# Kernel tuning notes

Measured on AMD Instinct MI355X. Metric: run time of the kernel, lower is better.

## Reference

```python
import jax, jax.numpy as jnp
import numpy as np

N = 50000          # number of input/output nodes (M == N since out_features=None)
E = 1_600_000      # total neighbor entries (avg degree 32)
C_IN = 64
HID = 128
C_OUT = 64


def setup_inputs() -> dict:
    key = jax.random.key(0)
    k1, k2, k3, k4, k5 = jax.random.split(key, 5)
    in_features = jax.random.normal(k1, (N, C_IN), dtype=jnp.float32)
    # MLP params: Linear(2C->HID), GELU, Linear(HID->C_OUT)
    W1 = jax.random.normal(k2, (2 * C_IN, HID), dtype=jnp.float32) * (1.0 / np.sqrt(2 * C_IN))
    b1 = jnp.zeros((HID,), dtype=jnp.float32)
    W2 = jax.random.normal(k3, (HID, C_OUT), dtype=jnp.float32) * (1.0 / np.sqrt(HID))
    b2 = jnp.zeros((C_OUT,), dtype=jnp.float32)
    neighbors_index = jax.random.randint(k4, (E,), 0, N, dtype=jnp.int64)
    # row_splits: sorted, starts at 0, ends at E (CSR-style ragged offsets)
    inner = jnp.sort(jax.random.randint(k5, (N - 1,), 0, E, dtype=jnp.int64))
    neighbors_row_splits = jnp.concatenate(
        [jnp.zeros((1,), jnp.int64), inner, jnp.full((1,), E, jnp.int64)])
    return {
        "in_features": in_features,
        "W1": W1, "b1": b1, "W2": W2, "b2": b2,
        "neighbors_index": neighbors_index,
        "neighbors_row_splits": neighbors_row_splits,
    }


def reference(in_features, W1, b1, W2, b2, neighbors_index, neighbors_row_splits):
    rs = neighbors_row_splits
    counts = rs[1:] - rs[:-1]                                  # [M] num_reps per row
    # segment id of each edge: row i owns edges [rs[i], rs[i+1])
    seg_ids = jnp.searchsorted(rs[1:], jnp.arange(E), side="right")  # [E]

    rep_features = in_features[neighbors_index]                # gather neighbors [E, C]
    self_features = in_features[seg_ids]                       # repeat_interleave  [E, C]
    agg = jnp.concatenate([rep_features, self_features], axis=1)  # [E, 2C]

    h = jax.nn.gelu(agg @ W1 + b1, approximate=False)          # torch GELU = exact erf
    msg = h @ W2 + b2                                          # [E, C_out]

    summed = jax.ops.segment_sum(msg, seg_ids, num_segments=N)  # [M, C_out]
    denom = jnp.maximum(counts, 1).astype(msg.dtype)[:, None]
    return summed / denom                                       # mean reduction
```

## Files before the change

### kernel.cpp

```cpp
#include <hip/hip_runtime.h>
#include <hip/hip_bf16.h>
#include <math.h>

#define C_IN  64
#define HID   128
#define C_OUT 64

typedef __attribute__((ext_vector_type(8))) short s16x8;
typedef __attribute__((ext_vector_type(4))) float f32x4;
typedef __attribute__((ext_vector_type(2))) float f32x2;

__device__ __forceinline__ f32x2 gelu2(f32x2 x) {
    f32x2 t  = x * x;
    f32x2 p  = t * 0.10294455f + 2.30211462f;
    f32x2 xp = x * p;
    f32x2 E;
    E.x = __builtin_amdgcn_exp2f(xp.x);
    E.y = __builtin_amdgcn_exp2f(xp.y);
    f32x2 Ep = E + 1.0f;
    f32x2 r;
    r.x = __builtin_amdgcn_rcpf(Ep.x);
    r.y = __builtin_amdgcn_rcpf(Ep.y);
    return x - x * r;
}

__device__ __forceinline__ float4 fma4(float s, float4 w, float4 acc) {
    acc.x = fmaf(s, w.x, acc.x); acc.y = fmaf(s, w.y, acc.y);
    acc.z = fmaf(s, w.z, acc.z); acc.w = fmaf(s, w.w, acc.w);
    return acc;
}

__device__ __forceinline__ unsigned pk_bf16(float lo, float hi) {
    union { __hip_bfloat162 v; unsigned u; } cv;
    cv.v = __float22bfloat162_rn(make_float2(lo, hi));
    return cv.u;
}
__device__ __forceinline__ f32x2 unpk2(unsigned p) {
    union { unsigned u; float f; } lo, hi;
    lo.u = p << 16; hi.u = p & 0xffff0000u;
    f32x2 v; v.x = lo.f; v.y = hi.f; return v;
}

#define K1_NODES 64

__global__ __launch_bounds__(512, 2) void precompute_ab(
    const float* __restrict__ X, const float* __restrict__ W1,
    const float* __restrict__ b1, const float* __restrict__ W2,
    const int* __restrict__ rs,
    unsigned* __restrict__ A16, float* __restrict__ B,
    unsigned short* __restrict__ W2T, int* __restrict__ bsplit,
    int N, int E, int G)
{
    __shared__ float W1s[2 * C_IN * HID];
    __shared__ float xs[K1_NODES * C_IN];
    int tid = threadIdx.x;

    for (int i = tid; i < (2 * C_IN * HID) / 4; i += 512)
        ((float4*)W1s)[i] = ((const float4*)W1)[i];

    int base = blockIdx.x * K1_NODES;
    int nLoc = min(K1_NODES, N - base);
    for (int i = tid; i < nLoc * (C_IN / 4); i += 512)
        ((float4*)xs)[i] = ((const float4*)(X + (size_t)base * C_IN))[i];

    if (blockIdx.x == 0) {
        for (int i = tid; i < C_OUT * HID; i += 512) {
            int c = i >> 7, k = i & (HID - 1);
            W2T[i] = (unsigned short)pk_bf16(W2[k * C_OUT + c], 0.f);
        }
    }

    {
        int gi = blockIdx.x * 512 + tid;
        if (gi <= G) {
            int t = (int)(((long long)E * gi) / G);
            int lo = 0, hi = N;
            while (lo < hi) { int mm = (lo + hi) >> 1; if (rs[mm] < t) lo = mm + 1; else hi = mm; }
            bsplit[gi] = lo;
        }
    }

    __syncthreads();

    int quad = (tid & 31) * 4;
    int slot = tid >> 5;
    int s0   = slot * 4;
    if (s0 >= nLoc) return;

    float4 a0 = {}, a1 = {}, a2 = {}, a3 = {};
    float4 b0 = {}, b1r = {}, b2r = {}, b3 = {};

    const float* xr0 = xs + (s0 + 0) * C_IN;
    const float* xr1 = xs + (s0 + 1) * C_IN;
    const float* xr2 = xs + (s0 + 2) * C_IN;
    const float* xr3 = xs + (s0 + 3) * C_IN;

#define K1STEP(c, CMP)                                                      \
    do {                                                                    \
        float4 wa = *(const float4*)&W1s[(c) * HID + quad];                 \
        float4 wb = *(const float4*)&W1s[((c) + C_IN) * HID + quad];        \
        a0 = fma4(xv0.CMP, wa, a0); b0  = fma4(xv0.CMP, wb, b0);            \
        a1 = fma4(xv1.CMP, wa, a1); b1r = fma4(xv1.CMP, wb, b1r);           \
        a2 = fma4(xv2.CMP, wa, a2); b2r = fma4(xv2.CMP, wb, b2r);           \
        a3 = fma4(xv3.CMP, wa, a3); b3  = fma4(xv3.CMP, wb, b3);            \
    } while (0)

#pragma unroll 1
    for (int c4 = 0; c4 < C_IN; c4 += 4) {
        float4 xv0 = *(const float4*)&xr0[c4];
        float4 xv1 = *(const float4*)&xr1[c4];
        float4 xv2 = *(const float4*)&xr2[c4];
        float4 xv3 = *(const float4*)&xr3[c4];
        K1STEP(c4 + 0, x);
        K1STEP(c4 + 1, y);
        K1STEP(c4 + 2, z);
        K1STEP(c4 + 3, w);
    }
#undef K1STEP

    float4 bb = *(const float4*)(b1 + quad);
    b0.x += bb.x;  b0.y += bb.y;  b0.z += bb.z;  b0.w += bb.w;
    b1r.x += bb.x; b1r.y += bb.y; b1r.z += bb.z; b1r.w += bb.w;
    b2r.x += bb.x; b2r.y += bb.y; b2r.z += bb.z; b2r.w += bb.w;
    b3.x += bb.x;  b3.y += bb.y;  b3.z += bb.z;  b3.w += bb.w;

    int adw = (base + s0) * (HID / 2) + (quad >> 1);
    size_t boff = (size_t)(base + s0) * HID + quad;
    if (s0 + 0 < nLoc) {
        uint2 u = { pk_bf16(a0.x, a0.y), pk_bf16(a0.z, a0.w) };
        *(uint2*)(A16 + adw) = u;              *(float4*)(B + boff) = b0;
    }
    if (s0 + 1 < nLoc) {
        uint2 u = { pk_bf16(a1.x, a1.y), pk_bf16(a1.z, a1.w) };
        *(uint2*)(A16 + adw + HID / 2) = u;    *(float4*)(B + boff + HID) = b1r;
    }
    if (s0 + 2 < nLoc) {
        uint2 u = { pk_bf16(a2.x, a2.y), pk_bf16(a2.z, a2.w) };
        *(uint2*)(A16 + adw + HID) = u;        *(float4*)(B + boff + 2 * HID) = b2r;
    }
    if (s0 + 3 < nLoc) {
        uint2 u = { pk_bf16(a3.x, a3.y), pk_bf16(a3.z, a3.w) };
        *(uint2*)(A16 + adw + 3 * (HID / 2)) = u; *(float4*)(B + boff + 3 * HID) = b3;
    }
}

#define EA_WAVES 2

#define EA_ISSUE(P0,P1,P2,P3, gc, IDX) do { int _b = ((gc) << 4) + q;         \
    int _i0 = __shfl((IDX), _b);                                              \
    int _i1 = __shfl((IDX), _b + 4);                                          \
    int _i2 = __shfl((IDX), _b + 8);                                          \
    int _i3 = __shfl((IDX), _b + 12);                                         \
    P0 = *(const uint4*)(A8 + ((((unsigned)_i0) << 8) | lb));                 \
    P1 = *(const uint4*)(A8 + ((((unsigned)_i1) << 8) | lb));                 \
    P2 = *(const uint4*)(A8 + ((((unsigned)_i2) << 8) | lb));                 \
    P3 = *(const uint4*)(A8 + ((((unsigned)_i3) << 8) | lb));                 \
} while (0)

#define EA_P1(P) do {                                                         \
    acc01 += gelu2(unpk2(P.x) + bb01);                                        \
    acc23 += gelu2(unpk2(P.y) + bb23);                                        \
    acc45 += gelu2(unpk2(P.z) + bb45);                                        \
    acc67 += gelu2(unpk2(P.w) + bb67); } while (0)

#define EA_P1M(P, eb) do {                                                    \
    float _mk = ((eb) + q < cnt) ? 1.f : 0.f;                                 \
    acc01 += gelu2(unpk2(P.x) + bb01) * _mk;                                  \
    acc23 += gelu2(unpk2(P.y) + bb23) * _mk;                                  \
    acc45 += gelu2(unpk2(P.z) + bb45) * _mk;                                  \
    acc67 += gelu2(unpk2(P.w) + bb67) * _mk; } while (0)

#define EA_PROCG(P0,P1,P2,P3, g) do {                                         \
    if ((((g) + 1) << 4) <= cnt) { EA_P1(P0); EA_P1(P1);                      \
                                   EA_P1(P2); EA_P1(P3); }                    \
    else { int _eb = (g) << 4;                                                \
           EA_P1M(P0, _eb);                                                   \
           if (_eb + 4  < cnt) EA_P1M(P1, _eb + 4);                           \
           if (_eb + 8  < cnt) EA_P1M(P2, _eb + 8);                           \
           if (_eb + 12 < cnt) EA_P1M(P3, _eb + 12); } } while (0)

__global__ __launch_bounds__(128, 6) void edge_agg(
    const unsigned* __restrict__ A16, const float* __restrict__ B,
    const int* __restrict__ nbr, const int* __restrict__ rs,
    const int* __restrict__ bsplit,
    unsigned* __restrict__ Hout, int N, int E, int G)
{
    int wave = threadIdx.x >> 6, lane = threadIdx.x & 63;
    int q  = lane >> 4;
    int l4 = lane & 15;
    const char* A8 = (const char*)A16;
    unsigned lb = (unsigned)(l4 << 4);
    int b = blockIdx.x;

    int r0 = bsplit[b];
    int r1 = (b == G - 1) ? N : bsplit[b + 1];

    int row = r0 + wave;
    if (row >= r1) return;

    int s = rs[row], e = rs[row + 1];
    int cnt = e - s;
    int idxCur = 0;
    if (cnt > 0) { int mn = min(64, cnt); idxCur = nbr[s + min(lane, mn - 1)]; }

    for (;;) {
        float4 bb4a = *(const float4*)(B + (size_t)row * HID + l4 * 8);
        float4 bb4b = *(const float4*)(B + (size_t)row * HID + l4 * 8 + 4);
        f32x2 bb01, bb23, bb45, bb67;
        bb01.x = bb4a.x; bb01.y = bb4a.y; bb23.x = bb4a.z; bb23.y = bb4a.w;
        bb45.x = bb4b.x; bb45.y = bb4b.y; bb67.x = bb4b.z; bb67.y = bb4b.w;
        f32x2 acc01 = {0.f, 0.f}, acc23 = {0.f, 0.f};
        f32x2 acc45 = {0.f, 0.f}, acc67 = {0.f, 0.f};

        uint4 A0, A1, A2, A3, B0, B1, B2, B3;
        int nG = 0, cLow = 0;
        int idxNxt = idxCur;
        if (cnt > 0) {
            nG = (cnt + 15) >> 4;
            EA_ISSUE(A0, A1, A2, A3, 0, idxCur);
            if (nG > 1) EA_ISSUE(B0, B1, B2, B3, 1, idxCur);
            if (cnt > 64) { int mn = min(64, cnt - 64);
                            idxNxt = nbr[s + 64 + min(lane, mn - 1)]; }
        }

        int nrow = row + EA_WAVES;
        bool hasn = nrow < r1;
        int sn = 0, cntn = 0, idxN0 = 0;
        if (hasn) {
            sn = rs[nrow]; int en = rs[nrow + 1]; cntn = en - sn;
            if (cntn > 0) { int mn = min(64, cntn);
                            idxN0 = nbr[sn + min(lane, mn - 1)]; }
        }

        if (cnt > 0) {
            int g = 0;
            for (;;) {
                EA_PROCG(A0, A1, A2, A3, g);
                { int gp = g + 2;
                  if (gp < nG) { int gc = gp & 3;
                      int IDX = ((gp >> 2) != cLow) ? idxNxt : idxCur;
                      EA_ISSUE(A0, A1, A2, A3, gc, IDX); } }
                if (++g >= nG) break;
                if ((g & 3) == 0) {
                    idxCur = idxNxt; ++cLow;
                    int nb = (cLow + 1) << 6;
                    if (nb < cnt) { int mn = min(64, cnt - nb);
                                    idxNxt = nbr[s + nb + min(lane, mn - 1)]; }
                }
                EA_PROCG(B0, B1, B2, B3, g);
                { int gp = g + 2;
                  if (gp < nG) { int gc = gp & 3;
                      int IDX = ((gp >> 2) != cLow) ? idxNxt : idxCur;
                      EA_ISSUE(B0, B1, B2, B3, gc, IDX); } }
                if (++g >= nG) break;
                if ((g & 3) == 0) {
                    idxCur = idxNxt; ++cLow;
                    int nb = (cLow + 1) << 6;
                    if (nb < cnt) { int mn = min(64, cnt - nb);
                                    idxNxt = nbr[s + nb + min(lane, mn - 1)]; }
                }
            }
        }

        acc01.x += __shfl_xor(acc01.x, 16); acc01.x += __shfl_xor(acc01.x, 32);
        acc01.y += __shfl_xor(acc01.y, 16); acc01.y += __shfl_xor(acc01.y, 32);
        acc23.x += __shfl_xor(acc23.x, 16); acc23.x += __shfl_xor(acc23.x, 32);
        acc23.y += __shfl_xor(acc23.y, 16); acc23.y += __shfl_xor(acc23.y, 32);
        acc45.x += __shfl_xor(acc45.x, 16); acc45.x += __shfl_xor(acc45.x, 32);
        acc45.y += __shfl_xor(acc45.y, 16); acc45.y += __shfl_xor(acc45.y, 32);
        acc67.x += __shfl_xor(acc67.x, 16); acc67.x += __shfl_xor(acc67.x, 32);
        acc67.y += __shfl_xor(acc67.y, 16); acc67.y += __shfl_xor(acc67.y, 32);

        if (q == 0) {
            float sc = (cnt > 0) ? 1.f / (float)cnt : 0.f;
            uint4 o;
            o.x = pk_bf16(acc01.x * sc, acc01.y * sc);
            o.y = pk_bf16(acc23.x * sc, acc23.y * sc);
            o.z = pk_bf16(acc45.x * sc, acc45.y * sc);
            o.w = pk_bf16(acc67.x * sc, acc67.y * sc);
            *((uint4*)(Hout + (size_t)row * (HID / 2)) + l4) = o;
        }

        if (!hasn) break;
        row = nrow; s = sn; cnt = cntn; idxCur = idxN0;
    }
}

#undef EA_ISSUE
#undef EA_P1
#undef EA_P1M
#undef EA_PROCG

__global__ __launch_bounds__(256) void h_w2_mfma(
    const unsigned short* __restrict__ H, const unsigned short* __restrict__ W2T,
    const float* __restrict__ b2, const int* __restrict__ rs,
    float* __restrict__ out, int N)
{
    int wave = threadIdx.x >> 6, lane = threadIdx.x & 63;
    int base = (blockIdx.x * 4 + wave) * 16;
    if (base >= N) return;

    int r16 = lane & 15;
    int kg  = lane >> 4;

    const unsigned short* hrow = H + (size_t)(base + r16) * HID + kg * 8;
    const unsigned short* wc0  = W2T + (size_t)(0 * 16 + r16) * HID + kg * 8;
    const unsigned short* wc1  = W2T + (size_t)(1 * 16 + r16) * HID + kg * 8;
    const unsigned short* wc2  = W2T + (size_t)(2 * 16 + r16) * HID + kg * 8;
    const unsigned short* wc3  = W2T + (size_t)(3 * 16 + r16) * HID + kg * 8;

    f32x4 acc0 = {0.f, 0.f, 0.f, 0.f};
    f32x4 acc1 = acc0, acc2 = acc0, acc3 = acc0;

#pragma unroll
    for (int kk = 0; kk < 4; ++kk) {
        s16x8 a  = *(const s16x8*)(hrow + kk * 32);
        s16x8 f0 = *(const s16x8*)(wc0 + kk * 32);
        s16x8 f1 = *(const s16x8*)(wc1 + kk * 32);
        s16x8 f2 = *(const s16x8*)(wc2 + kk * 32);
        s16x8 f3 = *(const s16x8*)(wc3 + kk * 32);
        acc0 = __builtin_amdgcn_mfma_f32_16x16x32_bf16(a, f0, acc0, 0, 0, 0);
        acc1 = __builtin_amdgcn_mfma_f32_16x16x32_bf16(a, f1, acc1, 0, 0, 0);
        acc2 = __builtin_amdgcn_mfma_f32_16x16x32_bf16(a, f2, acc2, 0, 0, 0);
        acc3 = __builtin_amdgcn_mfma_f32_16x16x32_bf16(a, f3, acc3, 0, 0, 0);
    }

    float bia0 = b2[r16], bia1 = b2[16 + r16], bia2 = b2[32 + r16], bia3 = b2[48 + r16];

#pragma unroll
    for (int r = 0; r < 4; ++r) {
        int rowi = base + kg * 4 + r;
        if (rowi < N) {
            float mmk = (rs[rowi + 1] > rs[rowi]) ? 1.f : 0.f;
            float* o = out + (size_t)rowi * C_OUT;
            o[r16]      = mmk * (acc0[r] + bia0);
            o[16 + r16] = mmk * (acc1[r] + bia1);
            o[32 + r16] = mmk * (acc2[r] + bia2);
            o[48 + r16] = mmk * (acc3[r] + bia3);
        }
    }
}

extern "C" void kernel_launch(void* const* d_in, const int* in_sizes, int n_in,
                              void* d_out, int out_size, void* d_ws, size_t ws_size,
                              hipStream_t stream) {
    const float* X  = (const float*)d_in[0];
    const float* W1 = (const float*)d_in[1];
    const float* b1 = (const float*)d_in[2];
    const float* W2 = (const float*)d_in[3];
    const float* b2 = (const float*)d_in[4];
    const int*   nbr = (const int*)d_in[5];
    const int*   rs  = (const int*)d_in[6];
    float* outp = (float*)d_out;

    int N = in_sizes[6] - 1;
    int E = in_sizes[5];

    int G = 3072;

    unsigned*       A16  = (unsigned*)d_ws;
    float*          Bbuf = (float*)(A16 + (size_t)N * (HID / 2));
    unsigned*       Hout = (unsigned*)(Bbuf + (size_t)N * HID);
    unsigned short* W2T  = (unsigned short*)(Hout + (size_t)N * (HID / 2));
    int*            bsplit = (int*)(W2T + C_OUT * HID);

    int g1 = (N + K1_NODES - 1) / K1_NODES;
    hipLaunchKernelGGL(precompute_ab, dim3(g1), dim3(512), 0, stream,
                       X, W1, b1, W2, rs, A16, Bbuf, W2T, bsplit, N, E, G);

    hipLaunchKernelGGL(edge_agg, dim3(G), dim3(128), 0, stream,
                       A16, Bbuf, nbr, rs, bsplit, Hout, N, E, G);

    int stripes = (N + 15) / 16;
    int g3 = (stripes + 3) / 4;
    hipLaunchKernelGGL(h_w2_mfma, dim3(g3), dim3(256), 0, stream,
                       (const unsigned short*)Hout, W2T, b2, rs, outp, N);
}
```

Before: 155.8 us.

## Split edge aggregation into four hidden-channel passes with planar A layout

Stores the bf16 A table as four planes of 32 hidden channels each and runs the edge aggregation as four launches, one per plane. Each pass gathers only 64 bytes per neighbor, so a plane's working set (about 3.2 MB) is more likely to stay cache-resident during random gathers. The pass also uses a three-buffer prefetch ring, nontemporal loads and stores, and a larger grid. The cost is that neighbor indices and row splits are re-read four times, there are extra launches, and each lane does fewer GELUs per load.

```diff
diff --git a/kernel.cpp b/kernel.cpp
--- a/kernel.cpp
+++ b/kernel.cpp
@@ -42,6 +42,7 @@
 }
 
 #define K1_NODES 64
+#define EA_G 6144
 
 __global__ __launch_bounds__(512, 2) void precompute_ab(
     const float* __restrict__ X, const float* __restrict__ W1,
@@ -124,7 +125,9 @@
     b2r.x += bb.x; b2r.y += bb.y; b2r.z += bb.z; b2r.w += bb.w;
     b3.x += bb.x;  b3.y += bb.y;  b3.z += bb.z;  b3.w += bb.w;
 
-    int adw = (base + s0) * (HID / 2) + (quad >> 1);
+    int pl = quad >> 5;
+    int d2 = quad & 31;
+    size_t adw = ((size_t)pl * N + (base + s0)) * 16 + (d2 >> 1);
     size_t boff = (size_t)(base + s0) * HID + quad;
     if (s0 + 0 < nLoc) {
         uint2 u = { pk_bf16(a0.x, a0.y), pk_bf16(a0.z, a0.w) };
@@ -132,64 +135,58 @@
     }
     if (s0 + 1 < nLoc) {
         uint2 u = { pk_bf16(a1.x, a1.y), pk_bf16(a1.z, a1.w) };
-        *(uint2*)(A16 + adw + HID / 2) = u;    *(float4*)(B + boff + HID) = b1r;
+        *(uint2*)(A16 + adw + 16) = u;         *(float4*)(B + boff + HID) = b1r;
     }
     if (s0 + 2 < nLoc) {
         uint2 u = { pk_bf16(a2.x, a2.y), pk_bf16(a2.z, a2.w) };
-        *(uint2*)(A16 + adw + HID) = u;        *(float4*)(B + boff + 2 * HID) = b2r;
+        *(uint2*)(A16 + adw + 32) = u;         *(float4*)(B + boff + 2 * HID) = b2r;
     }
     if (s0 + 3 < nLoc) {
         uint2 u = { pk_bf16(a3.x, a3.y), pk_bf16(a3.z, a3.w) };
-        *(uint2*)(A16 + adw + 3 * (HID / 2)) = u; *(float4*)(B + boff + 3 * HID) = b3;
+        *(uint2*)(A16 + adw + 48) = u;         *(float4*)(B + boff + 3 * HID) = b3;
     }
 }
 
 #define EA_WAVES 2
 
-#define EA_ISSUE(P0,P1,P2,P3, gc, IDX) do { int _b = ((gc) << 4) + q;         \
+#define EA_ISSUE(P0,P1,P2,P3, g, IDX) do { int _b = ((g) << 4) + q;           \
     int _i0 = __shfl((IDX), _b);                                              \
     int _i1 = __shfl((IDX), _b + 4);                                          \
     int _i2 = __shfl((IDX), _b + 8);                                          \
     int _i3 = __shfl((IDX), _b + 12);                                         \
-    P0 = *(const uint4*)(A8 + ((((unsigned)_i0) << 8) | lb));                 \
-    P1 = *(const uint4*)(A8 + ((((unsigned)_i1) << 8) | lb));                 \
-    P2 = *(const uint4*)(A8 + ((((unsigned)_i2) << 8) | lb));                 \
-    P3 = *(const uint4*)(A8 + ((((unsigned)_i3) << 8) | lb));                 \
+    P0 = *(const unsigned*)(Ap + ((((unsigned)_i0) << 6) | jb));              \
+    P1 = *(const unsigned*)(Ap + ((((unsigned)_i1) << 6) | jb));              \
+    P2 = *(const unsigned*)(Ap + ((((unsigned)_i2) << 6) | jb));              \
+    P3 = *(const unsigned*)(Ap + ((((unsigned)_i3) << 6) | jb));              \
 } while (0)
 
-#define EA_P1(P) do {                                                         \
-    acc01 += gelu2(unpk2(P.x) + bb01);                                        \
-    acc23 += gelu2(unpk2(P.y) + bb23);                                        \
-    acc45 += gelu2(unpk2(P.z) + bb45);                                        \
-    acc67 += gelu2(unpk2(P.w) + bb67); } while (0)
-
-#define EA_P1M(P, eb) do {                                                    \
-    float _mk = ((eb) + q < cnt) ? 1.f : 0.f;                                 \
-    acc01 += gelu2(unpk2(P.x) + bb01) * _mk;                                  \
-    acc23 += gelu2(unpk2(P.y) + bb23) * _mk;                                  \
-    acc45 += gelu2(unpk2(P.z) + bb45) * _mk;                                  \
-    acc67 += gelu2(unpk2(P.w) + bb67) * _mk; } while (0)
+#define EA_PF(P) do {                                                         \
+    acc += gelu2(unpk2(P) + bb); } while (0)
+
+#define EA_PM(P, eb) do {                                                     \
+    float _mk = ((eb) + q < m) ? 1.f : 0.f;                                   \
+    acc += gelu2(unpk2(P) + bb) * _mk; } while (0)
 
 #define EA_PROCG(P0,P1,P2,P3, g) do {                                         \
-    if ((((g) + 1) << 4) <= cnt) { EA_P1(P0); EA_P1(P1);                      \
-                                   EA_P1(P2); EA_P1(P3); }                    \
+    if ((((g) + 1) << 4) <= m) { EA_PF(P0); EA_PF(P1);                        \
+                                 EA_PF(P2); EA_PF(P3); }                      \
     else { int _eb = (g) << 4;                                                \
-           EA_P1M(P0, _eb);                                                   \
-           if (_eb + 4  < cnt) EA_P1M(P1, _eb + 4);                           \
-           if (_eb + 8  < cnt) EA_P1M(P2, _eb + 8);                           \
-           if (_eb + 12 < cnt) EA_P1M(P3, _eb + 12); } } while (0)
-
-__global__ __launch_bounds__(128, 6) void edge_agg(
+           EA_PM(P0, _eb);                                                    \
+           if (_eb + 4  < m) EA_PM(P1, _eb + 4);                              \
+           if (_eb + 8  < m) EA_PM(P2, _eb + 8);                              \
+           if (_eb + 12 < m) EA_PM(P3, _eb + 12); } } while (0)
+
+__global__ __launch_bounds__(128) void edge_agg_pass(
     const unsigned* __restrict__ A16, const float* __restrict__ B,
     const int* __restrict__ nbr, const int* __restrict__ rs,
     const int* __restrict__ bsplit,
-    unsigned* __restrict__ Hout, int N, int E, int G)
+    unsigned* __restrict__ Hout, int N, int E, int G, int pass)
 {
     int wave = threadIdx.x >> 6, lane = threadIdx.x & 63;
     int q  = lane >> 4;
-    int l4 = lane & 15;
-    const char* A8 = (const char*)A16;
-    unsigned lb = (unsigned)(l4 << 4);
+    int j  = lane & 15;
+    const char* Ap = (const char*)A16 + (size_t)pass * N * 64;
+    unsigned jb = (unsigned)(j << 2);
     int b = blockIdx.x;
 
     int r0 = bsplit[b];
@@ -201,94 +198,72 @@
     int s = rs[row], e = rs[row + 1];
     int cnt = e - s;
     int idxCur = 0;
-    if (cnt > 0) { int mn = min(64, cnt); idxCur = nbr[s + min(lane, mn - 1)]; }
+    if (cnt > 0) { int mn = min(64, cnt);
+                   idxCur = __builtin_nontemporal_load(nbr + s + min(lane, mn - 1)); }
 
     for (;;) {
-        float4 bb4a = *(const float4*)(B + (size_t)row * HID + l4 * 8);
-        float4 bb4b = *(const float4*)(B + (size_t)row * HID + l4 * 8 + 4);
-        f32x2 bb01, bb23, bb45, bb67;
-        bb01.x = bb4a.x; bb01.y = bb4a.y; bb23.x = bb4a.z; bb23.y = bb4a.w;
-        bb45.x = bb4b.x; bb45.y = bb4b.y; bb67.x = bb4b.z; bb67.y = bb4b.w;
-        f32x2 acc01 = {0.f, 0.f}, acc23 = {0.f, 0.f};
-        f32x2 acc45 = {0.f, 0.f}, acc67 = {0.f, 0.f};
-
-        uint4 A0, A1, A2, A3, B0, B1, B2, B3;
-        int nG = 0, cLow = 0;
-        int idxNxt = idxCur;
-        if (cnt > 0) {
-            nG = (cnt + 15) >> 4;
-            EA_ISSUE(A0, A1, A2, A3, 0, idxCur);
-            if (nG > 1) EA_ISSUE(B0, B1, B2, B3, 1, idxCur);
-            if (cnt > 64) { int mn = min(64, cnt - 64);
-                            idxNxt = nbr[s + 64 + min(lane, mn - 1)]; }
-        }
+        f32x2 bb = __builtin_nontemporal_load(
+            (const f32x2*)(B + (size_t)row * HID + (pass << 5) + (j << 1)));
+        f32x2 acc = {0.f, 0.f};
 
         int nrow = row + EA_WAVES;
         bool hasn = nrow < r1;
-        int sn = 0, cntn = 0, idxN0 = 0;
+        int sn = 0, en = 0, cntn = 0, idxN0 = 0;
         if (hasn) {
-            sn = rs[nrow]; int en = rs[nrow + 1]; cntn = en - sn;
+            sn = rs[nrow]; en = rs[nrow + 1]; cntn = en - sn;
             if (cntn > 0) { int mn = min(64, cntn);
-                            idxN0 = nbr[sn + min(lane, mn - 1)]; }
+                            idxN0 = __builtin_nontemporal_load(nbr + sn + min(lane, mn - 1)); }
         }
 
         if (cnt > 0) {
-            int g = 0;
+            int cs = s;
+            int idx = idxCur;
             for (;;) {
-                EA_PROCG(A0, A1, A2, A3, g);
-                { int gp = g + 2;
-                  if (gp < nG) { int gc = gp & 3;
-                      int IDX = ((gp >> 2) != cLow) ? idxNxt : idxCur;
-                      EA_ISSUE(A0, A1, A2, A3, gc, IDX); } }
-                if (++g >= nG) break;
-                if ((g & 3) == 0) {
-                    idxCur = idxNxt; ++cLow;
-                    int nb = (cLow + 1) << 6;
-                    if (nb < cnt) { int mn = min(64, cnt - nb);
-                                    idxNxt = nbr[s + nb + min(lane, mn - 1)]; }
+                int m = min(64, e - cs);
+                int nG = (m + 15) >> 4;
+
+                unsigned A0, A1, A2, A3, B0, B1, B2, B3, C0, C1, C2, C3;
+                EA_ISSUE(A0, A1, A2, A3, 0, idx);
+                if (nG > 1) EA_ISSUE(B0, B1, B2, B3, 1, idx);
+
+                int g = 0;
+                for (;;) {
+                    if (g + 2 < nG) EA_ISSUE(C0, C1, C2, C3, g + 2, idx);
+                    EA_PROCG(A0, A1, A2, A3, g);
+                    if (++g >= nG) break;
+                    if (g + 2 < nG) EA_ISSUE(A0, A1, A2, A3, g + 2, idx);
+                    EA_PROCG(B0, B1, B2, B3, g);
+                    if (++g >= nG) break;
+                    if (g + 2 < nG) EA_ISSUE(B0, B1, B2, B3, g + 2, idx);
+                    EA_PROCG(C0, C1, C2, C3, g);
+                    if (++g >= nG) break;
                 }
-                EA_PROCG(B0, B1, B2, B3, g);
-                { int gp = g + 2;
-                  if (gp < nG) { int gc = gp & 3;
-                      int IDX = ((gp >> 2) != cLow) ? idxNxt : idxCur;
-                      EA_ISSUE(B0, B1, B2, B3, gc, IDX); } }
-                if (++g >= nG) break;
-                if ((g & 3) == 0) {
-                    idxCur = idxNxt; ++cLow;
-                    int nb = (cLow + 1) << 6;
-                    if (nb < cnt) { int mn = min(64, cnt - nb);
-                                    idxNxt = nbr[s + nb + min(lane, mn - 1)]; }
-                }
+
+                cs += 64;
+                if (cs >= e) break;
+                int mn = min(64, e - cs);
+                idx = __builtin_nontemporal_load(nbr + cs + min(lane, mn - 1));
             }
         }
 
-        acc01.x += __shfl_xor(acc01.x, 16); acc01.x += __shfl_xor(acc01.x, 32);
-        acc01.y += __shfl_xor(acc01.y, 16); acc01.y += __shfl_xor(acc01.y, 32);
-        acc23.x += __shfl_xor(acc23.x, 16); acc23.x += __shfl_xor(acc23.x, 32);
-        acc23.y += __shfl_xor(acc23.y, 16); acc23.y += __shfl_xor(acc23.y, 32);
-        acc45.x += __shfl_xor(acc45.x, 16); acc45.x += __shfl_xor(acc45.x, 32);
-        acc45.y += __shfl_xor(acc45.y, 16); acc45.y += __shfl_xor(acc45.y, 32);
-        acc67.x += __shfl_xor(acc67.x, 16); acc67.x += __shfl_xor(acc67.x, 32);
-        acc67.y += __shfl_xor(acc67.y, 16); acc67.y += __shfl_xor(acc67.y, 32);
+        acc.x += __shfl_xor(acc.x, 16); acc.x += __shfl_xor(acc.x, 32);
+        acc.y += __shfl_xor(acc.y, 16); acc.y += __shfl_xor(acc.y, 32);
 
         if (q == 0) {
             float sc = (cnt > 0) ? 1.f / (float)cnt : 0.f;
-            uint4 o;
-            o.x = pk_bf16(acc01.x * sc, acc01.y * sc);
-            o.y = pk_bf16(acc23.x * sc, acc23.y * sc);
-            o.z = pk_bf16(acc45.x * sc, acc45.y * sc);
-            o.w = pk_bf16(acc67.x * sc, acc67.y * sc);
-            *((uint4*)(Hout + (size_t)row * (HID / 2)) + l4) = o;
+            unsigned o = pk_bf16(acc.x * sc, acc.y * sc);
+            __builtin_nontemporal_store(
+                o, Hout + (size_t)row * (HID / 2) + (pass << 4) + j);
         }
 
         if (!hasn) break;
-        row = nrow; s = sn; cnt = cntn; idxCur = idxN0;
+        row = nrow; s = sn; e = en; cnt = cntn; idxCur = idxN0;
     }
 }
 
 #undef EA_ISSUE
-#undef EA_P1
-#undef EA_P1M
+#undef EA_PF
+#undef EA_PM
 #undef EA_PROCG
 
 __global__ __launch_bounds__(256) void h_w2_mfma(
@@ -356,7 +331,7 @@
     int N = in_sizes[6] - 1;
     int E = in_sizes[5];
 
-    int G = 3072;
+    int G = EA_G;
 
     unsigned*       A16  = (unsigned*)d_ws;
     float*          Bbuf = (float*)(A16 + (size_t)N * (HID / 2));
@@ -368,8 +343,9 @@
     hipLaunchKernelGGL(precompute_ab, dim3(g1), dim3(512), 0, stream,
                        X, W1, b1, W2, rs, A16, Bbuf, W2T, bsplit, N, E, G);
 
-    hipLaunchKernelGGL(edge_agg, dim3(G), dim3(128), 0, stream,
-                       A16, Bbuf, nbr, rs, bsplit, Hout, N, E, G);
+    for (int p = 0; p < 4; ++p)
+        hipLaunchKernelGGL(edge_agg_pass, dim3(G), dim3(128), 0, stream,
+                           A16, Bbuf, nbr, rs, bsplit, Hout, N, E, G, p);
 
     int stripes = (N + 15) / 16;
     int g3 = (stripes + 3) / 4;
```

Measured after the change: 199.4 us. 27.9% more time.
